# Kernel tuning notes

Measured on AMD Instinct MI355X. Metric: run time of the kernel, lower is better.

Reference implementation:

```python
import jax, jax.numpy as jnp
import numpy as np

D_MODEL = 1024
H = 16
DK = D_MODEL // H  # 64
BLK = 128
TAU = 1.0
EPS = 1e-12


def setup_inputs() -> dict:
    key = jax.random.key(0)
    ks = jax.random.split(key, 5)
    B, N = 1, 2048
    shp = (B, N, D_MODEL)
    q = jax.random.normal(ks[0], shp, dtype=jnp.float32)
    k = jax.random.normal(ks[1], shp, dtype=jnp.float32)
    v = jax.random.normal(ks[2], shp, dtype=jnp.float32)
    dO = jax.random.normal(ks[3], shp, dtype=jnp.float32)
    Tb = N // BLK  # 16 blocks per side
    block_sparse_mask = jax.random.randint(ks[4], (Tb, Tb), 0, 2, dtype=jnp.int32)
    return {"q": q, "k": k, "v": v, "dO": dO, "block_sparse_mask": block_sparse_mask}


def reference(q, k, v, dO, block_sparse_mask):
    B, N, _ = q.shape
    T = N // BLK  # number of blocks along sequence
    scale = TAU / np.sqrt(DK).astype(np.float32)

    def split(x):
        # (B,N,d_model) -> (B,H,T,BLK,DK)
        return x.reshape(B, N, H, DK).transpose(0, 2, 1, 3).reshape(B, H, T, BLK, DK)

    qb, kb, vb, dOb = split(q), split(k), split(v), split(dO)

    # block scores: (B,H,Ti,Tj,Br,Bc)
    S = jnp.einsum('bhipd,bhjqd->bhijpq', qb, kb) * scale
    # per-block (local) softmax normalization, exactly as in the source
    m = jnp.max(S, axis=-1, keepdims=True)
    P = jnp.exp(S - m)
    l = jnp.sum(P, axis=-1, keepdims=True)
    Pn = P / (l + EPS)

    dA = jnp.einsum('bhipd,bhjqd->bhijpq', dOb, vb)
    row_dot = jnp.sum(dA * Pn, axis=-1, keepdims=True)
    dS = Pn * (dA - row_dot)

    # block-sparse skipping: skipped (i,j) blocks contribute nothing
    bm = block_sparse_mask.astype(Pn.dtype)[None, None, :, :, None, None]
    Pn = Pn * bm
    dS = dS * bm

    dV = jnp.einsum('bhijpq,bhipd->bhjqd', Pn, dOb)
    dQ = jnp.einsum('bhijpq,bhjqd->bhipd', dS, kb) * scale
    dK = jnp.einsum('bhijpq,bhipd->bhjqd', dS, qb) * scale

    def merge(x):
        # (B,H,T,BLK,DK) -> (B,N,d_model)
        return x.reshape(B, H, N, DK).transpose(0, 2, 1, 3).reshape(B, N, D_MODEL)

    return (merge(dQ), merge(dK), merge(dV))
```

## Files before the change

### kernel.cpp

```cpp
#include <hip/hip_runtime.h>
#include <hip/hip_bf16.h>

#define DMODEL 1024
#define NHEAD  16
#define DKD    64
#define BLK    128
#define TB     16
#define SCALEF 0.125f

typedef __attribute__((ext_vector_type(8))) short bf16x8;
typedef __attribute__((ext_vector_type(4))) _Float16 f16x4;
typedef __attribute__((ext_vector_type(4))) float f32x4;
typedef __attribute__((ext_vector_type(4))) unsigned int ui4;

#define MFMA(A, B, C)   __builtin_amdgcn_mfma_f32_16x16x32_bf16(A, B, C, 0, 0, 0)
#define MFMA16(A, B, C) __builtin_amdgcn_mfma_f32_16x16x16f16(A, B, C, 0, 0, 0)

union U8 { bf16x8 v; ushort u[8]; ushort2 u2[4]; ushort4 u4[2]; };

__device__ __forceinline__ ushort2 pk2(float a, float b) {
  union { __hip_bfloat162 h; ushort2 u; } c;
  c.h = __float22bfloat162_rn(make_float2(a, b));
  return c.u;
}
__device__ __forceinline__ ushort4 pkh4(float a, float b, float c, float d) {
  union { f16x4 h; ushort4 u; } z;
  z.h[0] = (_Float16)a; z.h[1] = (_Float16)b;
  z.h[2] = (_Float16)c; z.h[3] = (_Float16)d;
  return z.u;
}

__device__ __forceinline__ bf16x8 frag64(const ushort* T, int r, int c) {
  return *reinterpret_cast<const bf16x8*>(T + ((r * 64 + c) ^ ((r & 7) << 3)));
}
__device__ __forceinline__ bf16x8 frag64g(const ushort* T, int r, int c) {
  return __builtin_nontemporal_load(
      reinterpret_cast<const bf16x8*>(T + ((r * 64 + c) ^ ((r & 7) << 3))));
}
__device__ __forceinline__ bf16x8 frag128(const ushort* T, int r, int c) {
  return *reinterpret_cast<const bf16x8*>(T + ((r * 128 + c) ^ ((r & 7) << 3)));
}
__device__ __forceinline__ bf16x8 fragT2(const ushort* T, int d, int r0) {
  const int base = (r0 >> 2) * 256 + ((d * 4) ^ (((d >> 4) & 3) << 2));
  U8 x;
  x.u4[0] = *reinterpret_cast<const ushort4*>(T + base);
  x.u4[1] = *reinterpret_cast<const ushort4*>(T + base + 256);
  return x.v;
}
__device__ __forceinline__ f16x4 fragK16(const ushort* T, int d, int g) {
  union { ushort4 u; f16x4 h; } z;
  z.u = *reinterpret_cast<const ushort4*>(T + g * 256 + ((d * 4) ^ (((d >> 4) & 3) << 2)));
  return z.h;
}
__device__ __forceinline__ bf16x8 gfrag(const float* __restrict__ g, float sc) {
  const float4 fa = *reinterpret_cast<const float4*>(g);
  const float4 fb = *reinterpret_cast<const float4*>(g + 4);
  U8 x;
  x.u2[0] = pk2(fa.x * sc, fa.y * sc);
  x.u2[1] = pk2(fa.z * sc, fa.w * sc);
  x.u2[2] = pk2(fb.x * sc, fb.y * sc);
  x.u2[3] = pk2(fb.z * sc, fb.w * sc);
  return x.v;
}

__device__ __forceinline__ void gwrow(ushort* T, const float* __restrict__ g,
                                      float sc, int tid) {
#pragma unroll
  for (int it = 0; it < 4; ++it) {
    const int idx = tid + 512 * it;
    const int r = idx >> 4, d4 = idx & 15;
    const float4 f = *reinterpret_cast<const float4*>(g + r * DMODEL + 4 * d4);
    const ushort2 lo = pk2(f.x * sc, f.y * sc);
    const ushort2 hi = pk2(f.z * sc, f.w * sc);
    ushort4 u; u.x = lo.x; u.y = lo.y; u.z = hi.x; u.w = hi.y;
    *reinterpret_cast<ushort4*>(T + ((r * 64 + 4 * d4) ^ ((r & 7) << 3))) = u;
  }
}
template <int HALF>
__device__ __forceinline__ void gwchunk(ushort* T, const float* __restrict__ g,
                                        float sc, int tid) {
  const int a = (tid >> 4) & 3;
#pragma unroll
  for (int it = 0; it < 4; ++it) {
    const int idx = tid + 512 * it;
    const int r = idx >> 4, d4 = idx & 15;
    const float4 f = *reinterpret_cast<const float4*>(g + r * DMODEL + 4 * d4);
    const float w0 = f.x * sc, w1 = f.y * sc, w2 = f.z * sc, w3 = f.w * sc;
    const float s0 = __shfl_xor(w1, 16), s1 = __shfl_xor(w0, 16);
    const float s2 = __shfl_xor(w3, 16), s3 = __shfl_xor(w2, 16);
    const float u0 = (a & 1) ? s0 : w0;
    const float u1 = (a & 1) ? w1 : s1;
    const float u2 = (a & 1) ? s2 : w2;
    const float u3 = (a & 1) ? w3 : s3;
    const float t0 = __shfl_xor(u2, 32), t1 = __shfl_xor(u3, 32);
    const float t2 = __shfl_xor(u0, 32), t3 = __shfl_xor(u1, 32);
    const float z0 = (a & 2) ? t0 : u0;
    const float z1 = (a & 2) ? t1 : u1;
    const float z2 = (a & 2) ? u2 : t2;
    const float z3 = (a & 2) ? u3 : t3;
    const int d = 4 * d4 + a, R0 = r - a;
    ushort4 o;
    if constexpr (HALF) {
      o = pkh4(z0, z1, z2, z3);
    } else {
      const ushort2 lo = pk2(z0, z1);
      const ushort2 hi = pk2(z2, z3);
      o.x = lo.x; o.y = lo.y; o.z = hi.x; o.w = hi.y;
    }
    *reinterpret_cast<ushort4*>(T + (R0 >> 2) * 256 + ((d * 4) ^ (((d >> 4) & 3) << 2))) = o;
  }
}

__device__ __forceinline__ ushort* IMGp(ushort* ws, int imgN, int h, int t, int i) {
  return ws + (((size_t)h * TB + t) * imgN + i) * 8192;
}
__device__ __forceinline__ const ushort* IMGc(const ushort* ws, int imgN, int h, int t, int i) {
  return ws + (((size_t)h * TB + t) * imgN + i) * 8192;
}

__global__ void __launch_bounds__(512, 2)
prepass(const float* __restrict__ q, const float* __restrict__ kk,
        const float* __restrict__ v, const float* __restrict__ dOg,
        ushort* __restrict__ ws, int imgN) {
  const int bid = blockIdx.x;
  const int h = bid >> 4, t = bid & 15;
  const int tid = threadIdx.x;
  const size_t off = (size_t)(t * BLK) * DMODEL + h * DKD;
  gwrow     (IMGp(ws, imgN, h, t, 0), kk + off, SCALEF, tid);
  gwrow     (IMGp(ws, imgN, h, t, 1), v  + off, 1.f,    tid);
  gwchunk<1>(IMGp(ws, imgN, h, t, 2), kk + off, SCALEF, tid);
  gwchunk<0>(IMGp(ws, imgN, h, t, 3), q  + off, SCALEF, tid);
  gwchunk<0>(IMGp(ws, imgN, h, t, 4), dOg + off, 1.f,   tid);
  if (imgN >= 7) {
    gwrow(IMGp(ws, imgN, h, t, 5), q   + off, 1.f, tid);
    gwrow(IMGp(ws, imgN, h, t, 6), dOg + off, 1.f, tid);
  }
}

__device__ __forceinline__ void nt_issue(const ushort* src, int tid, ui4* r) {
  const ui4* s = reinterpret_cast<const ui4*>(src);
  r[0] = __builtin_nontemporal_load(s + tid);
  r[1] = __builtin_nontemporal_load(s + tid + 512);
}
__device__ __forceinline__ void lds_wr(ushort* dst, const ui4* r, int tid) {
  ui4* d = reinterpret_cast<ui4*>(dst);
  d[tid] = r[0];
  d[tid + 512] = r[1];
}

__global__ void __launch_bounds__(512, 1)
bwd_roles(const float* __restrict__ q, const float* __restrict__ dOg,
          const ushort* __restrict__ ws, const int* __restrict__ mask, int imgN,
          float* __restrict__ dQ, float* __restrict__ dK, float* __restrict__ dV) {
  __shared__ ushort sm[65536];
  const int tid = threadIdx.x;
  const int l = tid & 63, l15 = l & 15, lg = (l >> 4) & 3;
  const int w = tid >> 6, pw = w * 16;
  const int bid = blockIdx.x;
  const int xcd = bid & 7, idx = bid >> 3;
  const int h    = (xcd << 1) | (idx & 1);
  const int role = (idx >> 1) & 1;
  const int blk  = (idx >> 2) & 15;
  const f32x4 zz = {0.f, 0.f, 0.f, 0.f};

  if (role == 0) {
    unsigned bm = 0;
    for (int t = 0; t < TB; ++t)
      if (mask[blk * TB + t]) bm |= 1u << t;

    bf16x8 bq[2], bo[2];
#pragma unroll
    for (int kb = 0; kb < 2; ++kb) {
      const size_t row = (size_t)(blk * BLK + pw + l15) * DMODEL + h * DKD + kb * 32 + lg * 8;
      bq[kb] = gfrag(q + row, 1.f);
      bo[kb] = gfrag(dOg + row, 1.f);
    }
    f32x4 accQT[4] = {zz, zz, zz, zz};

    if (bm) {
      int j = __ffs(bm) - 1;
      unsigned rest = bm & (bm - 1);
      {
        ui4 t0[2], t1[2], t2[2];
        nt_issue(IMGc(ws, imgN, h, j, 0), tid, t0);
        nt_issue(IMGc(ws, imgN, h, j, 1), tid, t1);
        nt_issue(IMGc(ws, imgN, h, j, 2), tid, t2);
        lds_wr(sm + 0, t0, tid);
        lds_wr(sm + 8192, t1, tid);
        lds_wr(sm + 16384, t2, tid);
      }
      __syncthreads();
      int cur = 0;
      while (j >= 0) {
        const int jn = rest ? (__ffs(rest) - 1) : -1;
        rest = rest ? (rest & (rest - 1)) : 0u;
        ui4 pk0[2], pk1[2], pk2r[2];
        if (jn >= 0) {
          nt_issue(IMGc(ws, imgN, h, jn, 0), tid, pk0);
          nt_issue(IMGc(ws, imgN, h, jn, 1), tid, pk1);
          nt_issue(IMGc(ws, imgN, h, jn, 2), tid, pk2r);
        }
        const ushort* kR = sm + cur * 24576;
        const ushort* vR = sm + cur * 24576 + 8192;
        const ushort* kT = sm + cur * 24576 + 16384;

        f32x4 ST[8], dAT[8];
#pragma unroll
        for (int mf = 0; mf < 8; ++mf) { ST[mf] = zz; dAT[mf] = zz; }
#pragma unroll
        for (int kb = 0; kb < 2; ++kb) {
          const int ck = kb * 32 + lg * 8;
#pragma unroll
          for (int mf = 0; mf < 8; ++mf) {
            ST[mf]  = MFMA(frag64(kR, mf * 16 + l15, ck), bq[kb], ST[mf]);
            dAT[mf] = MFMA(frag64(vR, mf * 16 + l15, ck), bo[kb], dAT[mf]);
          }
        }
        float mx = -1e30f;
#pragma unroll
        for (int mf = 0; mf < 8; ++mf)
#pragma unroll
          for (int r = 0; r < 4; ++r) mx = fmaxf(mx, ST[mf][r]);
        mx = fmaxf(mx, __shfl_xor(mx, 16));
        mx = fmaxf(mx, __shfl_xor(mx, 32));
        float ss = 0.f;
#pragma unroll
        for (int mf = 0; mf < 8; ++mf)
#pragma unroll
          for (int r = 0; r < 4; ++r) { const float e = __expf(ST[mf][r] - mx); ST[mf][r] = e; ss += e; }
        ss += __shfl_xor(ss, 16);
        ss += __shfl_xor(ss, 32);
        const float inv = 1.f / (ss + 1e-12f);
        float rd = 0.f;
#pragma unroll
        for (int mf = 0; mf < 8; ++mf)
#pragma unroll
          for (int r = 0; r < 4; ++r) { const float pn = ST[mf][r] * inv; ST[mf][r] = pn; rd += pn * dAT[mf][r]; }
        rd += __shfl_xor(rd, 16);
        rd += __shfl_xor(rd, 32);

        f16x4 pb[8];
#pragma unroll
        for (int mf = 0; mf < 8; ++mf) {
#pragma unroll
          for (int r = 0; r < 4; ++r)
            pb[mf][r] = (_Float16)(ST[mf][r] * (dAT[mf][r] - rd));
        }
#pragma unroll
        for (int df = 0; df < 4; ++df)
#pragma unroll
          for (int mf = 0; mf < 8; ++mf)
            accQT[df] = MFMA16(fragK16(kT, df * 16 + l15, mf * 4 + lg), pb[mf], accQT[df]);

        if (jn >= 0) {
          ushort* nb = sm + (cur ^ 1) * 24576;
          lds_wr(nb, pk0, tid);
          lds_wr(nb + 8192, pk1, tid);
          lds_wr(nb + 16384, pk2r, tid);
        }
        __syncthreads();
        cur ^= 1;
        j = jn;
      }
    }
#pragma unroll
    for (int df = 0; df < 4; ++df) {
      f32x4 wv;
      wv[0] = accQT[df][0]; wv[1] = accQT[df][1];
      wv[2] = accQT[df][2]; wv[3] = accQT[df][3];
      __builtin_nontemporal_store(wv, reinterpret_cast<f32x4*>(
          dQ + (size_t)(blk * BLK + pw + l15) * DMODEL + h * DKD + df * 16 + lg * 4));
    }

  } else {
    const int jb = blk;
    unsigned bm = 0;
    for (int t = 0; t < TB; ++t)
      if (mask[t * TB + jb]) bm |= 1u << t;

    f32x4 accK[4] = {zz, zz, zz, zz};
    f32x4 accV[4] = {zz, zz, zz, zz};

    if (bm) {
      const bool hasR = (imgN >= 7);
      ushort* kR = sm;
      ushort* vR = sm + 8192;
      ushort* qT = sm + 16384;
      ushort* oT = sm + 24576;
      ushort* X1 = sm + 32768;
      ushort* X2 = sm + 49152;
      int i = __ffs(bm) - 1;
      unsigned rest = bm & (bm - 1);
      bf16x8 aq[2], ao[2];
      {
        ui4 t0[2], t1[2], t2[2], t3[2];
        nt_issue(IMGc(ws, imgN, h, jb, 0), tid, t0);
        nt_issue(IMGc(ws, imgN, h, jb, 1), tid, t1);
        nt_issue(IMGc(ws, imgN, h, i, 3), tid, t2);
        nt_issue(IMGc(ws, imgN, h, i, 4), tid, t3);
        lds_wr(kR, t0, tid);
        lds_wr(vR, t1, tid);
        lds_wr(qT, t2, tid);
        lds_wr(oT, t3, tid);
        if (hasR) {
#pragma unroll
          for (int kb = 0; kb < 2; ++kb) {
            aq[kb] = frag64g(IMGc(ws, imgN, h, i, 5), pw + l15, kb * 32 + lg * 8);
            ao[kb] = frag64g(IMGc(ws, imgN, h, i, 6), pw + l15, kb * 32 + lg * 8);
          }
        } else {
#pragma unroll
          for (int kb = 0; kb < 2; ++kb) {
            const size_t row = (size_t)(i * BLK + pw + l15) * DMODEL + h * DKD + kb * 32 + lg * 8;
            aq[kb] = gfrag(q + row, 1.f);
            ao[kb] = gfrag(dOg + row, 1.f);
          }
        }
      }
      __syncthreads();

      while (i >= 0) {
        const int in = rest ? (__ffs(rest) - 1) : -1;
        rest = rest ? (rest & (rest - 1)) : 0u;
        ui4 pq[2], po[2];
        bf16x8 nq[2], no[2];
        if (in >= 0) {
          nt_issue(IMGc(ws, imgN, h, in, 3), tid, pq);
          nt_issue(IMGc(ws, imgN, h, in, 4), tid, po);
          if (hasR) {
#pragma unroll
            for (int kb = 0; kb < 2; ++kb) {
              nq[kb] = frag64g(IMGc(ws, imgN, h, in, 5), pw + l15, kb * 32 + lg * 8);
              no[kb] = frag64g(IMGc(ws, imgN, h, in, 6), pw + l15, kb * 32 + lg * 8);
            }
          } else {
#pragma unroll
            for (int kb = 0; kb < 2; ++kb) {
              const size_t row = (size_t)(in * BLK + pw + l15) * DMODEL + h * DKD + kb * 32 + lg * 8;
              nq[kb] = gfrag(q + row, 1.f);
              no[kb] = gfrag(dOg + row, 1.f);
            }
          }
        }

        f32x4 S[8], dA[8];
#pragma unroll
        for (int nf = 0; nf < 8; ++nf) { S[nf] = zz; dA[nf] = zz; }
#pragma unroll
        for (int kb = 0; kb < 2; ++kb) {
          const int ck = kb * 32 + lg * 8;
#pragma unroll
          for (int nf = 0; nf < 8; ++nf) {
            S[nf]  = MFMA(aq[kb], frag64(kR, nf * 16 + l15, ck), S[nf]);
            dA[nf] = MFMA(ao[kb], frag64(vR, nf * 16 + l15, ck), dA[nf]);
          }
        }
#pragma unroll
        for (int r = 0; r < 4; ++r) {
          float mx = -1e30f;
#pragma unroll
          for (int nf = 0; nf < 8; ++nf) mx = fmaxf(mx, S[nf][r]);
          mx = fmaxf(mx, __shfl_xor(mx, 1));
          mx = fmaxf(mx, __shfl_xor(mx, 2));
          mx = fmaxf(mx, __shfl_xor(mx, 4));
          mx = fmaxf(mx, __shfl_xor(mx, 8));
          float ss = 0.f;
#pragma unroll
          for (int nf = 0; nf < 8; ++nf) { const float e = __expf(S[nf][r] - mx); S[nf][r] = e; ss += e; }
          ss += __shfl_xor(ss, 1); ss += __shfl_xor(ss, 2);
          ss += __shfl_xor(ss, 4); ss += __shfl_xor(ss, 8);
          const float inv = 1.f / (ss + 1e-12f);
          float rd = 0.f;
#pragma unroll
          for (int nf = 0; nf < 8; ++nf) { const float pn = S[nf][r] * inv; S[nf][r] = pn; rd += pn * dA[nf][r]; }
          rd += __shfl_xor(rd, 1); rd += __shfl_xor(rd, 2);
          rd += __shfl_xor(rd, 4); rd += __shfl_xor(rd, 8);
#pragma unroll
          for (int nf = 0; nf < 8; ++nf) dA[nf][r] = S[nf][r] * (dA[nf][r] - rd);
        }

#pragma unroll
        for (int nf = 0; nf < 8; ++nf) {
          const int c = nf * 16 + l15;
          const int off = (c * 128 + pw + 4 * lg) ^ ((c & 7) << 3);
          {
            const ushort2 lo = pk2(S[nf][0], S[nf][1]);
            const ushort2 hi = pk2(S[nf][2], S[nf][3]);
            ushort4 u; u.x = lo.x; u.y = lo.y; u.z = hi.x; u.w = hi.y;
            *reinterpret_cast<ushort4*>(X1 + off) = u;
          }
          {
            const ushort2 lo = pk2(dA[nf][0], dA[nf][1]);
            const ushort2 hi = pk2(dA[nf][2], dA[nf][3]);
            ushort4 u; u.x = lo.x; u.y = lo.y; u.z = hi.x; u.w = hi.y;
            *reinterpret_cast<ushort4*>(X2 + off) = u;
          }
        }
        __syncthreads();

#pragma unroll
        for (int kp = 0; kp < 4; ++kp) {
          const int pp = kp * 32 + lg * 8;
          const bf16x8 a1 = frag128(X1, pw + l15, pp);
          const bf16x8 a2 = frag128(X2, pw + l15, pp);
#pragma unroll
          for (int nfd = 0; nfd < 4; ++nfd) {
            accV[nfd] = MFMA(a1, fragT2(oT, nfd * 16 + l15, pp), accV[nfd]);
            accK[nfd] = MFMA(a2, fragT2(qT, nfd * 16 + l15, pp), accK[nfd]);
          }
        }
        __syncthreads();

        if (in >= 0) {
          lds_wr(qT, pq, tid);
          lds_wr(oT, po, tid);
          aq[0] = nq[0]; aq[1] = nq[1];
          ao[0] = no[0]; ao[1] = no[1];
        }
        i = in;
      }
    }
#pragma unroll
    for (int nfd = 0; nfd < 4; ++nfd)
#pragma unroll
      for (int r = 0; r < 4; ++r) {
        const size_t rowo = (size_t)(jb * BLK + pw + lg * 4 + r) * DMODEL + h * DKD + nfd * 16 + l15;
        __builtin_nontemporal_store(accK[nfd][r], &dK[rowo]);
        __builtin_nontemporal_store(accV[nfd][r], &dV[rowo]);
      }
  }
}

extern "C" void kernel_launch(void* const* d_in, const int* in_sizes, int n_in,
                              void* d_out, int out_size, void* d_ws, size_t ws_size,
                              hipStream_t stream) {
  const float* q  = (const float*)d_in[0];
  const float* k  = (const float*)d_in[1];
  const float* v  = (const float*)d_in[2];
  const float* dO = (const float*)d_in[3];
  const int* mask = (const int*)d_in[4];
  float* out = (float*)d_out;
  float* dQ = out;
  float* dK = out + (size_t)2048 * DMODEL;
  float* dV = out + (size_t)2 * 2048 * DMODEL;
  ushort* ws = (ushort*)d_ws;

  const size_t need7 = (size_t)NHEAD * TB * 7 * 16384;
  const int imgN = (ws_size >= need7) ? 7 : 5;

  prepass<<<NHEAD * TB, 512, 0, stream>>>(q, k, v, dO, ws, imgN);
  bwd_roles<<<2 * NHEAD * TB, 512, 0, stream>>>(q, dO, ws, mask, imgN, dQ, dK, dV);
}
```

Before: 119.7 us.

## Halve LDS footprint to raise occupancy, drop double buffering, relayout transposed tiles

Shared memory per block is cut from 128KB to 64KB and launch bounds raised to 4 waves/SIMD target, so more blocks can be resident per CU. To fit, the role-0 loop drops its double-buffered K/V/KT tiles in favour of single buffers refilled between barriers. The role-1 loop reuses one scratch region X for both P and dS in sequence and reloads K/V into LDS because X aliases them. The transposed tile layout also changes to 8-wide contiguous groups so each fragment is one 16-byte load instead of two 8-byte loads. The trade is extra barriers, redundant K/V reloads each iteration and less prefetch overlap, in exchange for higher occupancy.

```diff
diff --git a/kernel.cpp b/kernel.cpp
--- a/kernel.cpp
+++ b/kernel.cpp
@@ -40,16 +40,12 @@
 __device__ __forceinline__ bf16x8 frag128(const ushort* T, int r, int c) {
   return *reinterpret_cast<const bf16x8*>(T + ((r * 128 + c) ^ ((r & 7) << 3)));
 }
-__device__ __forceinline__ bf16x8 fragT2(const ushort* T, int d, int r0) {
-  const int base = (r0 >> 2) * 256 + ((d * 4) ^ (((d >> 4) & 3) << 2));
-  U8 x;
-  x.u4[0] = *reinterpret_cast<const ushort4*>(T + base);
-  x.u4[1] = *reinterpret_cast<const ushort4*>(T + base + 256);
-  return x.v;
+__device__ __forceinline__ bf16x8 fragT8(const ushort* T, int d, int r0) {
+  return *reinterpret_cast<const bf16x8*>(T + (r0 >> 3) * 512 + d * 8);
 }
 __device__ __forceinline__ f16x4 fragK16(const ushort* T, int d, int g) {
   union { ushort4 u; f16x4 h; } z;
-  z.u = *reinterpret_cast<const ushort4*>(T + g * 256 + ((d * 4) ^ (((d >> 4) & 3) << 2)));
+  z.u = *reinterpret_cast<const ushort4*>(T + (g >> 1) * 512 + d * 8 + 4 * (g & 1));
   return z.h;
 }
 __device__ __forceinline__ bf16x8 gfrag(const float* __restrict__ g, float sc) {
@@ -107,7 +103,7 @@
       const ushort2 hi = pk2(z2, z3);
       o.x = lo.x; o.y = lo.y; o.z = hi.x; o.w = hi.y;
     }
-    *reinterpret_cast<ushort4*>(T + (R0 >> 2) * 256 + ((d * 4) ^ (((d >> 4) & 3) << 2))) = o;
+    *reinterpret_cast<ushort4*>(T + (R0 >> 3) * 512 + d * 8 + (R0 & 7)) = o;
   }
 }
 
@@ -148,11 +144,11 @@
   d[tid + 512] = r[1];
 }
 
-__global__ void __launch_bounds__(512, 1)
+__global__ void __launch_bounds__(512, 4)
 bwd_roles(const float* __restrict__ q, const float* __restrict__ dOg,
           const ushort* __restrict__ ws, const int* __restrict__ mask, int imgN,
           float* __restrict__ dQ, float* __restrict__ dK, float* __restrict__ dV) {
-  __shared__ ushort sm[65536];
+  __shared__ ushort sm[32768];
   const int tid = threadIdx.x;
   const int l = tid & 63, l15 = l & 15, lg = (l >> 4) & 3;
   const int w = tid >> 6, pw = w * 16;
@@ -164,6 +160,9 @@
   const f32x4 zz = {0.f, 0.f, 0.f, 0.f};
 
   if (role == 0) {
+    ushort* kR = sm;
+    ushort* vR = sm + 8192;
+    ushort* kT = sm + 16384;
     unsigned bm = 0;
     for (int t = 0; t < TB; ++t)
       if (mask[blk * TB + t]) bm |= 1u << t;
@@ -185,12 +184,11 @@
         nt_issue(IMGc(ws, imgN, h, j, 0), tid, t0);
         nt_issue(IMGc(ws, imgN, h, j, 1), tid, t1);
         nt_issue(IMGc(ws, imgN, h, j, 2), tid, t2);
-        lds_wr(sm + 0, t0, tid);
-        lds_wr(sm + 8192, t1, tid);
-        lds_wr(sm + 16384, t2, tid);
+        lds_wr(kR, t0, tid);
+        lds_wr(vR, t1, tid);
+        lds_wr(kT, t2, tid);
       }
       __syncthreads();
-      int cur = 0;
       while (j >= 0) {
         const int jn = rest ? (__ffs(rest) - 1) : -1;
         rest = rest ? (rest & (rest - 1)) : 0u;
@@ -200,9 +198,6 @@
           nt_issue(IMGc(ws, imgN, h, jn, 1), tid, pk1);
           nt_issue(IMGc(ws, imgN, h, jn, 2), tid, pk2r);
         }
-        const ushort* kR = sm + cur * 24576;
-        const ushort* vR = sm + cur * 24576 + 8192;
-        const ushort* kT = sm + cur * 24576 + 16384;
 
         f32x4 ST[8], dAT[8];
 #pragma unroll
@@ -241,25 +236,23 @@
 
         f16x4 pb[8];
 #pragma unroll
-        for (int mf = 0; mf < 8; ++mf) {
+        for (int mf = 0; mf < 8; ++mf)
 #pragma unroll
           for (int r = 0; r < 4; ++r)
             pb[mf][r] = (_Float16)(ST[mf][r] * (dAT[mf][r] - rd));
+
+        __syncthreads();
+        if (jn >= 0) {
+          lds_wr(kR, pk0, tid);
+          lds_wr(vR, pk1, tid);
         }
 #pragma unroll
         for (int df = 0; df < 4; ++df)
 #pragma unroll
           for (int mf = 0; mf < 8; ++mf)
             accQT[df] = MFMA16(fragK16(kT, df * 16 + l15, mf * 4 + lg), pb[mf], accQT[df]);
-
-        if (jn >= 0) {
-          ushort* nb = sm + (cur ^ 1) * 24576;
-          lds_wr(nb, pk0, tid);
-          lds_wr(nb + 8192, pk1, tid);
-          lds_wr(nb + 16384, pk2r, tid);
-        }
-        __syncthreads();
-        cur ^= 1;
+        __syncthreads();
+        if (jn >= 0) lds_wr(kT, pk2r, tid);
         j = jn;
       }
     }
@@ -273,6 +266,11 @@
     }
 
   } else {
+    ushort* kR = sm;
+    ushort* vR = sm + 8192;
+    ushort* qT = sm + 16384;
+    ushort* oT = sm + 24576;
+    ushort* X  = sm;
     const int jb = blk;
     unsigned bm = 0;
     for (int t = 0; t < TB; ++t)
@@ -283,15 +281,8 @@
 
     if (bm) {
       const bool hasR = (imgN >= 7);
-      ushort* kR = sm;
-      ushort* vR = sm + 8192;
-      ushort* qT = sm + 16384;
-      ushort* oT = sm + 24576;
-      ushort* X1 = sm + 32768;
-      ushort* X2 = sm + 49152;
       int i = __ffs(bm) - 1;
       unsigned rest = bm & (bm - 1);
-      bf16x8 aq[2], ao[2];
       {
         ui4 t0[2], t1[2], t2[2], t3[2];
         nt_issue(IMGc(ws, imgN, h, jb, 0), tid, t0);
@@ -302,6 +293,14 @@
         lds_wr(vR, t1, tid);
         lds_wr(qT, t2, tid);
         lds_wr(oT, t3, tid);
+      }
+      __syncthreads();
+
+      while (i >= 0) {
+        const int in = rest ? (__ffs(rest) - 1) : -1;
+        rest = rest ? (rest & (rest - 1)) : 0u;
+
+        bf16x8 aq[2], ao[2];
         if (hasR) {
 #pragma unroll
           for (int kb = 0; kb < 2; ++kb) {
@@ -314,32 +313,6 @@
             const size_t row = (size_t)(i * BLK + pw + l15) * DMODEL + h * DKD + kb * 32 + lg * 8;
             aq[kb] = gfrag(q + row, 1.f);
             ao[kb] = gfrag(dOg + row, 1.f);
-          }
-        }
-      }
-      __syncthreads();
-
-      while (i >= 0) {
-        const int in = rest ? (__ffs(rest) - 1) : -1;
-        rest = rest ? (rest & (rest - 1)) : 0u;
-        ui4 pq[2], po[2];
-        bf16x8 nq[2], no[2];
-        if (in >= 0) {
-          nt_issue(IMGc(ws, imgN, h, in, 3), tid, pq);
-          nt_issue(IMGc(ws, imgN, h, in, 4), tid, po);
-          if (hasR) {
-#pragma unroll
-            for (int kb = 0; kb < 2; ++kb) {
-              nq[kb] = frag64g(IMGc(ws, imgN, h, in, 5), pw + l15, kb * 32 + lg * 8);
-              no[kb] = frag64g(IMGc(ws, imgN, h, in, 6), pw + l15, kb * 32 + lg * 8);
-            }
-          } else {
-#pragma unroll
-            for (int kb = 0; kb < 2; ++kb) {
-              const size_t row = (size_t)(in * BLK + pw + l15) * DMODEL + h * DKD + kb * 32 + lg * 8;
-              nq[kb] = gfrag(q + row, 1.f);
-              no[kb] = gfrag(dOg + row, 1.f);
-            }
           }
         }
 
@@ -378,44 +351,64 @@
 #pragma unroll
           for (int nf = 0; nf < 8; ++nf) dA[nf][r] = S[nf][r] * (dA[nf][r] - rd);
         }
+        __syncthreads();
 
 #pragma unroll
         for (int nf = 0; nf < 8; ++nf) {
           const int c = nf * 16 + l15;
           const int off = (c * 128 + pw + 4 * lg) ^ ((c & 7) << 3);
-          {
-            const ushort2 lo = pk2(S[nf][0], S[nf][1]);
-            const ushort2 hi = pk2(S[nf][2], S[nf][3]);
-            ushort4 u; u.x = lo.x; u.y = lo.y; u.z = hi.x; u.w = hi.y;
-            *reinterpret_cast<ushort4*>(X1 + off) = u;
-          }
-          {
-            const ushort2 lo = pk2(dA[nf][0], dA[nf][1]);
-            const ushort2 hi = pk2(dA[nf][2], dA[nf][3]);
-            ushort4 u; u.x = lo.x; u.y = lo.y; u.z = hi.x; u.w = hi.y;
-            *reinterpret_cast<ushort4*>(X2 + off) = u;
-          }
+          const ushort2 lo = pk2(S[nf][0], S[nf][1]);
+          const ushort2 hi = pk2(S[nf][2], S[nf][3]);
+          ushort4 u; u.x = lo.x; u.y = lo.y; u.z = hi.x; u.w = hi.y;
+          *reinterpret_cast<ushort4*>(X + off) = u;
         }
         __syncthreads();
 
 #pragma unroll
         for (int kp = 0; kp < 4; ++kp) {
           const int pp = kp * 32 + lg * 8;
-          const bf16x8 a1 = frag128(X1, pw + l15, pp);
-          const bf16x8 a2 = frag128(X2, pw + l15, pp);
-#pragma unroll
-          for (int nfd = 0; nfd < 4; ++nfd) {
-            accV[nfd] = MFMA(a1, fragT2(oT, nfd * 16 + l15, pp), accV[nfd]);
-            accK[nfd] = MFMA(a2, fragT2(qT, nfd * 16 + l15, pp), accK[nfd]);
-          }
-        }
-        __syncthreads();
-
+          const bf16x8 a = frag128(X, pw + l15, pp);
+#pragma unroll
+          for (int nfd = 0; nfd < 4; ++nfd)
+            accV[nfd] = MFMA(a, fragT8(oT, nfd * 16 + l15, pp), accV[nfd]);
+        }
+        __syncthreads();
+
+        ui4 pk0[2], pk1[2], pq[2], po[2];
         if (in >= 0) {
+          nt_issue(IMGc(ws, imgN, h, jb, 0), tid, pk0);
+          nt_issue(IMGc(ws, imgN, h, jb, 1), tid, pk1);
+          nt_issue(IMGc(ws, imgN, h, in, 3), tid, pq);
+          nt_issue(IMGc(ws, imgN, h, in, 4), tid, po);
+        }
+
+#pragma unroll
+        for (int nf = 0; nf < 8; ++nf) {
+          const int c = nf * 16 + l15;
+          const int off = (c * 128 + pw + 4 * lg) ^ ((c & 7) << 3);
+          const ushort2 lo = pk2(dA[nf][0], dA[nf][1]);
+          const ushort2 hi = pk2(dA[nf][2], dA[nf][3]);
+          ushort4 u; u.x = lo.x; u.y = lo.y; u.z = hi.x; u.w = hi.y;
+          *reinterpret_cast<ushort4*>(X + off) = u;
+        }
+        __syncthreads();
+
+#pragma unroll
+        for (int kp = 0; kp < 4; ++kp) {
+          const int pp = kp * 32 + lg * 8;
+          const bf16x8 a = frag128(X, pw + l15, pp);
+#pragma unroll
+          for (int nfd = 0; nfd < 4; ++nfd)
+            accK[nfd] = MFMA(a, fragT8(qT, nfd * 16 + l15, pp), accK[nfd]);
+        }
+        __syncthreads();
+
+        if (in >= 0) {
+          lds_wr(kR, pk0, tid);
+          lds_wr(vR, pk1, tid);
           lds_wr(qT, pq, tid);
           lds_wr(oT, po, tid);
-          aq[0] = nq[0]; aq[1] = nq[1];
-          ao[0] = no[0]; ao[1] = no[1];
+          __syncthreads();
         }
         i = in;
       }
```

Result: slower. 244.5 us (+104.2%).

## Split mask loop across two workgroups with atomic accumulation and MFMA priority

Applied to the files above, without the earlier changes.

Doubles the grid so each output tile is handled by two workgroups, each taking alternate mask blocks (even or odd). Partial dQ/dK/dV are combined with float atomicAdd into an output that a memset zeroes first. Workgroups with an empty mask subset now exit early. MFMA sections are wrapped in s_setprio to favour matrix issue. The change raises parallelism and balances load, at the cost of atomic traffic, an extra memset, and a summation order that can vary between runs.

```diff
diff --git a/kernel.cpp b/kernel.cpp
--- a/kernel.cpp
+++ b/kernel.cpp
@@ -161,12 +161,14 @@
   const int h    = (xcd << 1) | (idx & 1);
   const int role = (idx >> 1) & 1;
   const int blk  = (idx >> 2) & 15;
+  const int par  = (idx >> 6) & 1;
   const f32x4 zz = {0.f, 0.f, 0.f, 0.f};
 
   if (role == 0) {
     unsigned bm = 0;
-    for (int t = 0; t < TB; ++t)
+    for (int t = par; t < TB; t += 2)
       if (mask[blk * TB + t]) bm |= 1u << t;
+    if (!bm) return;
 
     bf16x8 bq[2], bo[2];
 #pragma unroll
@@ -177,256 +179,259 @@
     }
     f32x4 accQT[4] = {zz, zz, zz, zz};
 
-    if (bm) {
-      int j = __ffs(bm) - 1;
-      unsigned rest = bm & (bm - 1);
-      {
-        ui4 t0[2], t1[2], t2[2];
-        nt_issue(IMGc(ws, imgN, h, j, 0), tid, t0);
-        nt_issue(IMGc(ws, imgN, h, j, 1), tid, t1);
-        nt_issue(IMGc(ws, imgN, h, j, 2), tid, t2);
-        lds_wr(sm + 0, t0, tid);
-        lds_wr(sm + 8192, t1, tid);
-        lds_wr(sm + 16384, t2, tid);
+    int j = __ffs(bm) - 1;
+    unsigned rest = bm & (bm - 1);
+    {
+      ui4 t0[2], t1[2], t2[2];
+      nt_issue(IMGc(ws, imgN, h, j, 0), tid, t0);
+      nt_issue(IMGc(ws, imgN, h, j, 1), tid, t1);
+      nt_issue(IMGc(ws, imgN, h, j, 2), tid, t2);
+      lds_wr(sm + 0, t0, tid);
+      lds_wr(sm + 8192, t1, tid);
+      lds_wr(sm + 16384, t2, tid);
+    }
+    __syncthreads();
+    int cur = 0;
+    while (j >= 0) {
+      const int jn = rest ? (__ffs(rest) - 1) : -1;
+      rest = rest ? (rest & (rest - 1)) : 0u;
+      ui4 pk0[2], pk1[2], pk2r[2];
+      if (jn >= 0) {
+        nt_issue(IMGc(ws, imgN, h, jn, 0), tid, pk0);
+        nt_issue(IMGc(ws, imgN, h, jn, 1), tid, pk1);
+        nt_issue(IMGc(ws, imgN, h, jn, 2), tid, pk2r);
+      }
+      const ushort* kR = sm + cur * 24576;
+      const ushort* vR = sm + cur * 24576 + 8192;
+      const ushort* kT = sm + cur * 24576 + 16384;
+
+      f32x4 ST[8], dAT[8];
+#pragma unroll
+      for (int mf = 0; mf < 8; ++mf) { ST[mf] = zz; dAT[mf] = zz; }
+      __builtin_amdgcn_s_setprio(1);
+#pragma unroll
+      for (int kb = 0; kb < 2; ++kb) {
+        const int ck = kb * 32 + lg * 8;
+#pragma unroll
+        for (int mf = 0; mf < 8; ++mf) {
+          ST[mf]  = MFMA(frag64(kR, mf * 16 + l15, ck), bq[kb], ST[mf]);
+          dAT[mf] = MFMA(frag64(vR, mf * 16 + l15, ck), bo[kb], dAT[mf]);
+        }
+      }
+      __builtin_amdgcn_s_setprio(0);
+      float mx = -1e30f;
+#pragma unroll
+      for (int mf = 0; mf < 8; ++mf)
+#pragma unroll
+        for (int r = 0; r < 4; ++r) mx = fmaxf(mx, ST[mf][r]);
+      mx = fmaxf(mx, __shfl_xor(mx, 16));
+      mx = fmaxf(mx, __shfl_xor(mx, 32));
+      float ss = 0.f;
+#pragma unroll
+      for (int mf = 0; mf < 8; ++mf)
+#pragma unroll
+        for (int r = 0; r < 4; ++r) { const float e = __expf(ST[mf][r] - mx); ST[mf][r] = e; ss += e; }
+      ss += __shfl_xor(ss, 16);
+      ss += __shfl_xor(ss, 32);
+      const float inv = 1.f / (ss + 1e-12f);
+      float rd = 0.f;
+#pragma unroll
+      for (int mf = 0; mf < 8; ++mf)
+#pragma unroll
+        for (int r = 0; r < 4; ++r) { const float pn = ST[mf][r] * inv; ST[mf][r] = pn; rd += pn * dAT[mf][r]; }
+      rd += __shfl_xor(rd, 16);
+      rd += __shfl_xor(rd, 32);
+
+      f16x4 pb[8];
+#pragma unroll
+      for (int mf = 0; mf < 8; ++mf) {
+#pragma unroll
+        for (int r = 0; r < 4; ++r)
+          pb[mf][r] = (_Float16)(ST[mf][r] * (dAT[mf][r] - rd));
+      }
+      __builtin_amdgcn_s_setprio(1);
+#pragma unroll
+      for (int df = 0; df < 4; ++df)
+#pragma unroll
+        for (int mf = 0; mf < 8; ++mf)
+          accQT[df] = MFMA16(fragK16(kT, df * 16 + l15, mf * 4 + lg), pb[mf], accQT[df]);
+      __builtin_amdgcn_s_setprio(0);
+
+      if (jn >= 0) {
+        ushort* nb = sm + (cur ^ 1) * 24576;
+        lds_wr(nb, pk0, tid);
+        lds_wr(nb + 8192, pk1, tid);
+        lds_wr(nb + 16384, pk2r, tid);
       }
       __syncthreads();
-      int cur = 0;
-      while (j >= 0) {
-        const int jn = rest ? (__ffs(rest) - 1) : -1;
-        rest = rest ? (rest & (rest - 1)) : 0u;
-        ui4 pk0[2], pk1[2], pk2r[2];
-        if (jn >= 0) {
-          nt_issue(IMGc(ws, imgN, h, jn, 0), tid, pk0);
-          nt_issue(IMGc(ws, imgN, h, jn, 1), tid, pk1);
-          nt_issue(IMGc(ws, imgN, h, jn, 2), tid, pk2r);
-        }
-        const ushort* kR = sm + cur * 24576;
-        const ushort* vR = sm + cur * 24576 + 8192;
-        const ushort* kT = sm + cur * 24576 + 16384;
-
-        f32x4 ST[8], dAT[8];
-#pragma unroll
-        for (int mf = 0; mf < 8; ++mf) { ST[mf] = zz; dAT[mf] = zz; }
-#pragma unroll
-        for (int kb = 0; kb < 2; ++kb) {
-          const int ck = kb * 32 + lg * 8;
-#pragma unroll
-          for (int mf = 0; mf < 8; ++mf) {
-            ST[mf]  = MFMA(frag64(kR, mf * 16 + l15, ck), bq[kb], ST[mf]);
-            dAT[mf] = MFMA(frag64(vR, mf * 16 + l15, ck), bo[kb], dAT[mf]);
-          }
-        }
-        float mx = -1e30f;
-#pragma unroll
-        for (int mf = 0; mf < 8; ++mf)
-#pragma unroll
-          for (int r = 0; r < 4; ++r) mx = fmaxf(mx, ST[mf][r]);
-        mx = fmaxf(mx, __shfl_xor(mx, 16));
-        mx = fmaxf(mx, __shfl_xor(mx, 32));
-        float ss = 0.f;
-#pragma unroll
-        for (int mf = 0; mf < 8; ++mf)
-#pragma unroll
-          for (int r = 0; r < 4; ++r) { const float e = __expf(ST[mf][r] - mx); ST[mf][r] = e; ss += e; }
-        ss += __shfl_xor(ss, 16);
-        ss += __shfl_xor(ss, 32);
-        const float inv = 1.f / (ss + 1e-12f);
-        float rd = 0.f;
-#pragma unroll
-        for (int mf = 0; mf < 8; ++mf)
-#pragma unroll
-          for (int r = 0; r < 4; ++r) { const float pn = ST[mf][r] * inv; ST[mf][r] = pn; rd += pn * dAT[mf][r]; }
-        rd += __shfl_xor(rd, 16);
-        rd += __shfl_xor(rd, 32);
-
-        f16x4 pb[8];
-#pragma unroll
-        for (int mf = 0; mf < 8; ++mf) {
-#pragma unroll
-          for (int r = 0; r < 4; ++r)
-            pb[mf][r] = (_Float16)(ST[mf][r] * (dAT[mf][r] - rd));
-        }
-#pragma unroll
-        for (int df = 0; df < 4; ++df)
-#pragma unroll
-          for (int mf = 0; mf < 8; ++mf)
-            accQT[df] = MFMA16(fragK16(kT, df * 16 + l15, mf * 4 + lg), pb[mf], accQT[df]);
-
-        if (jn >= 0) {
-          ushort* nb = sm + (cur ^ 1) * 24576;
-          lds_wr(nb, pk0, tid);
-          lds_wr(nb + 8192, pk1, tid);
-          lds_wr(nb + 16384, pk2r, tid);
-        }
-        __syncthreads();
-        cur ^= 1;
-        j = jn;
-      }
+      cur ^= 1;
+      j = jn;
     }
 #pragma unroll
     for (int df = 0; df < 4; ++df) {
-      f32x4 wv;
-      wv[0] = accQT[df][0]; wv[1] = accQT[df][1];
-      wv[2] = accQT[df][2]; wv[3] = accQT[df][3];
-      __builtin_nontemporal_store(wv, reinterpret_cast<f32x4*>(
-          dQ + (size_t)(blk * BLK + pw + l15) * DMODEL + h * DKD + df * 16 + lg * 4));
+      float* base = dQ + (size_t)(blk * BLK + pw + l15) * DMODEL + h * DKD + df * 16 + lg * 4;
+#pragma unroll
+      for (int r = 0; r < 4; ++r) atomicAdd(base + r, accQT[df][r]);
     }
 
   } else {
     const int jb = blk;
     unsigned bm = 0;
-    for (int t = 0; t < TB; ++t)
+    for (int t = par; t < TB; t += 2)
       if (mask[t * TB + jb]) bm |= 1u << t;
+    if (!bm) return;
 
     f32x4 accK[4] = {zz, zz, zz, zz};
     f32x4 accV[4] = {zz, zz, zz, zz};
 
-    if (bm) {
-      const bool hasR = (imgN >= 7);
-      ushort* kR = sm;
-      ushort* vR = sm + 8192;
-      ushort* qT = sm + 16384;
-      ushort* oT = sm + 24576;
-      ushort* X1 = sm + 32768;
-      ushort* X2 = sm + 49152;
-      int i = __ffs(bm) - 1;
-      unsigned rest = bm & (bm - 1);
-      bf16x8 aq[2], ao[2];
-      {
-        ui4 t0[2], t1[2], t2[2], t3[2];
-        nt_issue(IMGc(ws, imgN, h, jb, 0), tid, t0);
-        nt_issue(IMGc(ws, imgN, h, jb, 1), tid, t1);
-        nt_issue(IMGc(ws, imgN, h, i, 3), tid, t2);
-        nt_issue(IMGc(ws, imgN, h, i, 4), tid, t3);
-        lds_wr(kR, t0, tid);
-        lds_wr(vR, t1, tid);
-        lds_wr(qT, t2, tid);
-        lds_wr(oT, t3, tid);
+    const bool hasR = (imgN >= 7);
+    ushort* kR = sm;
+    ushort* vR = sm + 8192;
+    ushort* qT = sm + 16384;
+    ushort* oT = sm + 24576;
+    ushort* X1 = sm + 32768;
+    ushort* X2 = sm + 49152;
+    int i = __ffs(bm) - 1;
+    unsigned rest = bm & (bm - 1);
+    bf16x8 aq[2], ao[2];
+    {
+      ui4 t0[2], t1[2], t2[2], t3[2];
+      nt_issue(IMGc(ws, imgN, h, jb, 0), tid, t0);
+      nt_issue(IMGc(ws, imgN, h, jb, 1), tid, t1);
+      nt_issue(IMGc(ws, imgN, h, i, 3), tid, t2);
+      nt_issue(IMGc(ws, imgN, h, i, 4), tid, t3);
+      lds_wr(kR, t0, tid);
+      lds_wr(vR, t1, tid);
+      lds_wr(qT, t2, tid);
+      lds_wr(oT, t3, tid);
+      if (hasR) {
+#pragma unroll
+        for (int kb = 0; kb < 2; ++kb) {
+          aq[kb] = frag64g(IMGc(ws, imgN, h, i, 5), pw + l15, kb * 32 + lg * 8);
+          ao[kb] = frag64g(IMGc(ws, imgN, h, i, 6), pw + l15, kb * 32 + lg * 8);
+        }
+      } else {
+#pragma unroll
+        for (int kb = 0; kb < 2; ++kb) {
+          const size_t row = (size_t)(i * BLK + pw + l15) * DMODEL + h * DKD + kb * 32 + lg * 8;
+          aq[kb] = gfrag(q + row, 1.f);
+          ao[kb] = gfrag(dOg + row, 1.f);
+        }
+      }
+    }
+    __syncthreads();
+
+    while (i >= 0) {
+      const int in = rest ? (__ffs(rest) - 1) : -1;
+      rest = rest ? (rest & (rest - 1)) : 0u;
+      ui4 pq[2], po[2];
+      bf16x8 nq[2], no[2];
+      if (in >= 0) {
+        nt_issue(IMGc(ws, imgN, h, in, 3), tid, pq);
+        nt_issue(IMGc(ws, imgN, h, in, 4), tid, po);
         if (hasR) {
 #pragma unroll
           for (int kb = 0; kb < 2; ++kb) {
-            aq[kb] = frag64g(IMGc(ws, imgN, h, i, 5), pw + l15, kb * 32 + lg * 8);
-            ao[kb] = frag64g(IMGc(ws, imgN, h, i, 6), pw + l15, kb * 32 + lg * 8);
+            nq[kb] = frag64g(IMGc(ws, imgN, h, in, 5), pw + l15, kb * 32 + lg * 8);
+            no[kb] = frag64g(IMGc(ws, imgN, h, in, 6), pw + l15, kb * 32 + lg * 8);
           }
         } else {
 #pragma unroll
           for (int kb = 0; kb < 2; ++kb) {
-            const size_t row = (size_t)(i * BLK + pw + l15) * DMODEL + h * DKD + kb * 32 + lg * 8;
-            aq[kb] = gfrag(q + row, 1.f);
-            ao[kb] = gfrag(dOg + row, 1.f);
+            const size_t row = (size_t)(in * BLK + pw + l15) * DMODEL + h * DKD + kb * 32 + lg * 8;
+            nq[kb] = gfrag(q + row, 1.f);
+            no[kb] = gfrag(dOg + row, 1.f);
           }
         }
       }
+
+      f32x4 S[8], dA[8];
+#pragma unroll
+      for (int nf = 0; nf < 8; ++nf) { S[nf] = zz; dA[nf] = zz; }
+      __builtin_amdgcn_s_setprio(1);
+#pragma unroll
+      for (int kb = 0; kb < 2; ++kb) {
+        const int ck = kb * 32 + lg * 8;
+#pragma unroll
+        for (int nf = 0; nf < 8; ++nf) {
+          S[nf]  = MFMA(aq[kb], frag64(kR, nf * 16 + l15, ck), S[nf]);
+          dA[nf] = MFMA(ao[kb], frag64(vR, nf * 16 + l15, ck), dA[nf]);
+        }
+      }
+      __builtin_amdgcn_s_setprio(0);
+#pragma unroll
+      for (int r = 0; r < 4; ++r) {
+        float mx = -1e30f;
+#pragma unroll
+        for (int nf = 0; nf < 8; ++nf) mx = fmaxf(mx, S[nf][r]);
+        mx = fmaxf(mx, __shfl_xor(mx, 1));
+        mx = fmaxf(mx, __shfl_xor(mx, 2));
+        mx = fmaxf(mx, __shfl_xor(mx, 4));
+        mx = fmaxf(mx, __shfl_xor(mx, 8));
+        float ss = 0.f;
+#pragma unroll
+        for (int nf = 0; nf < 8; ++nf) { const float e = __expf(S[nf][r] - mx); S[nf][r] = e; ss += e; }
+        ss += __shfl_xor(ss, 1); ss += __shfl_xor(ss, 2);
+        ss += __shfl_xor(ss, 4); ss += __shfl_xor(ss, 8);
+        const float inv = 1.f / (ss + 1e-12f);
+        float rd = 0.f;
+#pragma unroll
+        for (int nf = 0; nf < 8; ++nf) { const float pn = S[nf][r] * inv; S[nf][r] = pn; rd += pn * dA[nf][r]; }
+        rd += __shfl_xor(rd, 1); rd += __shfl_xor(rd, 2);
+        rd += __shfl_xor(rd, 4); rd += __shfl_xor(rd, 8);
+#pragma unroll
+        for (int nf = 0; nf < 8; ++nf) dA[nf][r] = S[nf][r] * (dA[nf][r] - rd);
+      }
+
+#pragma unroll
+      for (int nf = 0; nf < 8; ++nf) {
+        const int c = nf * 16 + l15;
+        const int off = (c * 128 + pw + 4 * lg) ^ ((c & 7) << 3);
+        {
+          const ushort2 lo = pk2(S[nf][0], S[nf][1]);
+          const ushort2 hi = pk2(S[nf][2], S[nf][3]);
+          ushort4 u; u.x = lo.x; u.y = lo.y; u.z = hi.x; u.w = hi.y;
+          *reinterpret_cast<ushort4*>(X1 + off) = u;
+        }
+        {
+          const ushort2 lo = pk2(dA[nf][0], dA[nf][1]);
+          const ushort2 hi = pk2(dA[nf][2], dA[nf][3]);
+          ushort4 u; u.x = lo.x; u.y = lo.y; u.z = hi.x; u.w = hi.y;
+          *reinterpret_cast<ushort4*>(X2 + off) = u;
+        }
+      }
       __syncthreads();
 
-      while (i >= 0) {
-        const int in = rest ? (__ffs(rest) - 1) : -1;
-        rest = rest ? (rest & (rest - 1)) : 0u;
-        ui4 pq[2], po[2];
-        bf16x8 nq[2], no[2];
-        if (in >= 0) {
-          nt_issue(IMGc(ws, imgN, h, in, 3), tid, pq);
-          nt_issue(IMGc(ws, imgN, h, in, 4), tid, po);
-          if (hasR) {
-#pragma unroll
-            for (int kb = 0; kb < 2; ++kb) {
-              nq[kb] = frag64g(IMGc(ws, imgN, h, in, 5), pw + l15, kb * 32 + lg * 8);
-              no[kb] = frag64g(IMGc(ws, imgN, h, in, 6), pw + l15, kb * 32 + lg * 8);
-            }
-          } else {
-#pragma unroll
-            for (int kb = 0; kb < 2; ++kb) {
-              const size_t row = (size_t)(in * BLK + pw + l15) * DMODEL + h * DKD + kb * 32 + lg * 8;
-              nq[kb] = gfrag(q + row, 1.f);
-              no[kb] = gfrag(dOg + row, 1.f);
-            }
-          }
-        }
-
-        f32x4 S[8], dA[8];
-#pragma unroll
-        for (int nf = 0; nf < 8; ++nf) { S[nf] = zz; dA[nf] = zz; }
-#pragma unroll
-        for (int kb = 0; kb < 2; ++kb) {
-          const int ck = kb * 32 + lg * 8;
-#pragma unroll
-          for (int nf = 0; nf < 8; ++nf) {
-            S[nf]  = MFMA(aq[kb], frag64(kR, nf * 16 + l15, ck), S[nf]);
-            dA[nf] = MFMA(ao[kb], frag64(vR, nf * 16 + l15, ck), dA[nf]);
-          }
-        }
-#pragma unroll
-        for (int r = 0; r < 4; ++r) {
-          float mx = -1e30f;
-#pragma unroll
-          for (int nf = 0; nf < 8; ++nf) mx = fmaxf(mx, S[nf][r]);
-          mx = fmaxf(mx, __shfl_xor(mx, 1));
-          mx = fmaxf(mx, __shfl_xor(mx, 2));
-          mx = fmaxf(mx, __shfl_xor(mx, 4));
-          mx = fmaxf(mx, __shfl_xor(mx, 8));
-          float ss = 0.f;
-#pragma unroll
-          for (int nf = 0; nf < 8; ++nf) { const float e = __expf(S[nf][r] - mx); S[nf][r] = e; ss += e; }
-          ss += __shfl_xor(ss, 1); ss += __shfl_xor(ss, 2);
-          ss += __shfl_xor(ss, 4); ss += __shfl_xor(ss, 8);
-          const float inv = 1.f / (ss + 1e-12f);
-          float rd = 0.f;
-#pragma unroll
-          for (int nf = 0; nf < 8; ++nf) { const float pn = S[nf][r] * inv; S[nf][r] = pn; rd += pn * dA[nf][r]; }
-          rd += __shfl_xor(rd, 1); rd += __shfl_xor(rd, 2);
-          rd += __shfl_xor(rd, 4); rd += __shfl_xor(rd, 8);
-#pragma unroll
-          for (int nf = 0; nf < 8; ++nf) dA[nf][r] = S[nf][r] * (dA[nf][r] - rd);
-        }
-
-#pragma unroll
-        for (int nf = 0; nf < 8; ++nf) {
-          const int c = nf * 16 + l15;
-          const int off = (c * 128 + pw + 4 * lg) ^ ((c & 7) << 3);
-          {
-            const ushort2 lo = pk2(S[nf][0], S[nf][1]);
-            const ushort2 hi = pk2(S[nf][2], S[nf][3]);
-            ushort4 u; u.x = lo.x; u.y = lo.y; u.z = hi.x; u.w = hi.y;
-            *reinterpret_cast<ushort4*>(X1 + off) = u;
-          }
-          {
-            const ushort2 lo = pk2(dA[nf][0], dA[nf][1]);
-            const ushort2 hi = pk2(dA[nf][2], dA[nf][3]);
-            ushort4 u; u.x = lo.x; u.y = lo.y; u.z = hi.x; u.w = hi.y;
-            *reinterpret_cast<ushort4*>(X2 + off) = u;
-          }
-        }
-        __syncthreads();
-
-#pragma unroll
-        for (int kp = 0; kp < 4; ++kp) {
-          const int pp = kp * 32 + lg * 8;
-          const bf16x8 a1 = frag128(X1, pw + l15, pp);
-          const bf16x8 a2 = frag128(X2, pw + l15, pp);
-#pragma unroll
-          for (int nfd = 0; nfd < 4; ++nfd) {
-            accV[nfd] = MFMA(a1, fragT2(oT, nfd * 16 + l15, pp), accV[nfd]);
-            accK[nfd] = MFMA(a2, fragT2(qT, nfd * 16 + l15, pp), accK[nfd]);
-          }
-        }
-        __syncthreads();
-
-        if (in >= 0) {
-          lds_wr(qT, pq, tid);
-          lds_wr(oT, po, tid);
-          aq[0] = nq[0]; aq[1] = nq[1];
-          ao[0] = no[0]; ao[1] = no[1];
-        }
-        i = in;
-      }
+      __builtin_amdgcn_s_setprio(1);
+#pragma unroll
+      for (int kp = 0; kp < 4; ++kp) {
+        const int pp = kp * 32 + lg * 8;
+        const bf16x8 a1 = frag128(X1, pw + l15, pp);
+        const bf16x8 a2 = frag128(X2, pw + l15, pp);
+#pragma unroll
+        for (int nfd = 0; nfd < 4; ++nfd) {
+          accV[nfd] = MFMA(a1, fragT2(oT, nfd * 16 + l15, pp), accV[nfd]);
+          accK[nfd] = MFMA(a2, fragT2(qT, nfd * 16 + l15, pp), accK[nfd]);
+        }
+      }
+      __builtin_amdgcn_s_setprio(0);
+      __syncthreads();
+
+      if (in >= 0) {
+        lds_wr(qT, pq, tid);
+        lds_wr(oT, po, tid);
+        aq[0] = nq[0]; aq[1] = nq[1];
+        ao[0] = no[0]; ao[1] = no[1];
+      }
+      i = in;
     }
 #pragma unroll
     for (int nfd = 0; nfd < 4; ++nfd)
 #pragma unroll
       for (int r = 0; r < 4; ++r) {
         const size_t rowo = (size_t)(jb * BLK + pw + lg * 4 + r) * DMODEL + h * DKD + nfd * 16 + l15;
-        __builtin_nontemporal_store(accK[nfd][r], &dK[rowo]);
-        __builtin_nontemporal_store(accV[nfd][r], &dV[rowo]);
+        atomicAdd(&dK[rowo], accK[nfd][r]);
+        atomicAdd(&dV[rowo], accV[nfd][r]);
       }
   }
 }
@@ -448,6 +453,7 @@
   const size_t need7 = (size_t)NHEAD * TB * 7 * 16384;
   const int imgN = (ws_size >= need7) ? 7 : 5;
 
+  hipMemsetAsync(d_out, 0, (size_t)out_size * sizeof(float), stream);
   prepass<<<NHEAD * TB, 512, 0, stream>>>(q, k, v, dO, ws, imgN);
-  bwd_roles<<<2 * NHEAD * TB, 512, 0, stream>>>(q, dO, ws, mask, imgN, dQ, dK, dV);
-}
+  bwd_roles<<<4 * NHEAD * TB, 512, 0, stream>>>(q, dO, ws, mask, imgN, dQ, dK, dV);
+}
```

Result: slower. 134.2 us (+12.1%).
